# Kernel optimization log

Measured on AMD Instinct MI355X. Metric: run time of the kernel, lower is better.

The kernel has to match this reference:

```python
import math
import jax, jax.numpy as jnp
import numpy as np

SAMPLE_RATE = 24000
HARMONIC_NUM = 8
SINE_AMP = 0.1


def setup_inputs() -> dict:
    key = jax.random.key(0)
    k1, k2, k3 = jax.random.split(key, 3)
    f0 = jax.random.uniform(k1, (32, 800), dtype=jnp.float32)  # frame-rate F0
    W = jax.random.normal(k2, (9, 1), dtype=jnp.float32) * (1.0 / 3.0)  # Linear(9,1) weight
    b = jax.random.normal(k3, (1,), dtype=jnp.float32) * 0.01
    return {"f0": f0, "W": W, "b": b, "upp": 240}


def reference(f0, W, b, upp):
    # nearest-neighbor upsample by integer factor upp == repeat each frame
    f0_up = jnp.repeat(f0, upp, axis=1)  # [batch, samples]
    batch, samples = f0_up.shape
    # harmonic multipliers h = 1..harmonic_num+1 (9 harmonics)
    h = jnp.arange(1, HARMONIC_NUM + 2, dtype=f0.dtype)  # [9]
    # cumsum(f0_up * h) == cumsum(f0_up) * h (cumsum is linear); one scan for all harmonics
    base_phase = jnp.cumsum(f0_up / SAMPLE_RATE, axis=1)  # [batch, samples]
    phase = base_phase[:, :, None] * (h * (2.0 * math.pi))  # [batch, samples, 9]
    sine = jnp.sin(phase) * SINE_AMP
    uv = (f0_up > 0).astype(f0.dtype)[:, :, None]  # [batch, samples, 1]
    harmonics = sine * uv
    har_source = jnp.tanh(harmonics @ W + b)  # [batch, samples, 1]
    noise = jax.random.normal(jax.random.key(1234), (batch, samples, 1), dtype=f0.dtype) * (SINE_AMP / 3.0)
    return (har_source, noise, uv)
```

## Files before the change

### kernel.cpp

```cpp
#include <hip/hip_runtime.h>
#include <stdint.h>

#define FRAMES  800
#define UPP     240
#define SAMPLES (FRAMES * UPP)
#define BATCH   32
#define NTOT    (BATCH * SAMPLES)
#define NHALF   (NTOT / 2)

#define THREEFRY_PARTITIONABLE 1

__device__ __forceinline__ uint32_t rotl32(uint32_t v, int d) {
  return (v << d) | (v >> (32 - d));
}

__device__ __forceinline__ void threefry2x32(uint32_t k0, uint32_t k1,
                                             uint32_t x0, uint32_t x1,
                                             uint32_t& o0, uint32_t& o1) {
  const uint32_t ks0 = k0, ks1 = k1, ks2 = k0 ^ k1 ^ 0x1BD11BDAu;
  x0 += ks0; x1 += ks1;
#define TF_R(r) { x0 += x1; x1 = rotl32(x1, r); x1 ^= x0; }
  TF_R(13) TF_R(15) TF_R(26) TF_R(6)   x0 += ks1; x1 += ks2 + 1u;
  TF_R(17) TF_R(29) TF_R(16) TF_R(24)  x0 += ks2; x1 += ks0 + 2u;
  TF_R(13) TF_R(15) TF_R(26) TF_R(6)   x0 += ks0; x1 += ks1 + 3u;
  TF_R(17) TF_R(29) TF_R(16) TF_R(24)  x0 += ks1; x1 += ks2 + 4u;
  TF_R(13) TF_R(15) TF_R(26) TF_R(6)   x0 += ks2; x1 += ks0 + 5u;
#undef TF_R
  o0 = x0; o1 = x1;
}

__device__ __forceinline__ float erfinv_f32(float x) {
  float w = -log1pf(-x * x);
  float p;
  if (w < 5.0f) {
    w = w - 2.5f;
    p = 2.81022636e-08f;
    p = fmaf(p, w, 3.43273939e-07f);
    p = fmaf(p, w, -3.5233877e-06f);
    p = fmaf(p, w, -4.39150654e-06f);
    p = fmaf(p, w, 0.00021858087f);
    p = fmaf(p, w, -0.00125372503f);
    p = fmaf(p, w, -0.00417768164f);
    p = fmaf(p, w, 0.246640727f);
    p = fmaf(p, w, 1.50140941f);
  } else {
    w = sqrtf(w) - 3.0f;
    p = -0.000200214257f;
    p = fmaf(p, w, 0.000100950558f);
    p = fmaf(p, w, 0.00134934322f);
    p = fmaf(p, w, -0.00367342844f);
    p = fmaf(p, w, 0.00573950773f);
    p = fmaf(p, w, -0.0076224613f);
    p = fmaf(p, w, 0.00943887047f);
    p = fmaf(p, w, 1.00167406f);
    p = fmaf(p, w, 2.83297682f);
  }
  return p * x;
}

__device__ __forceinline__ float bits_to_noise(uint32_t bits) {
  float f = __uint_as_float((bits >> 9) | 0x3f800000u);
  float u = f - 1.0f;
  const float lo = -0.99999994f;
  float val = fmaf(u, 2.0f, lo);
  val = fmaxf(lo, val);
  float n = 1.41421356f * erfinv_f32(val);
  return n * 0.033333335f;
}

#if THREEFRY_PARTITIONABLE
__global__ __launch_bounds__(256) void noise_kernel(float* __restrict__ out) {
  uint32_t i0 = (blockIdx.x * 256u + threadIdx.x) * 4u;
  if (i0 >= (uint32_t)NTOT) return;
  float4 r;
  uint32_t a, b;
  threefry2x32(0u, 1234u, 0u, i0 + 0u, a, b); r.x = bits_to_noise(a ^ b);
  threefry2x32(0u, 1234u, 0u, i0 + 1u, a, b); r.y = bits_to_noise(a ^ b);
  threefry2x32(0u, 1234u, 0u, i0 + 2u, a, b); r.z = bits_to_noise(a ^ b);
  threefry2x32(0u, 1234u, 0u, i0 + 3u, a, b); r.w = bits_to_noise(a ^ b);
  *(float4*)(out + i0) = r;
}
#else
__global__ __launch_bounds__(256) void noise_kernel(float* __restrict__ out) {
  uint32_t p0 = (blockIdx.x * 256u + threadIdx.x) * 4u;
  if (p0 >= (uint32_t)NHALF) return;
  float4 rlo, rhi;
  uint32_t a, b;
  threefry2x32(0u, 1234u, p0 + 0u, p0 + 0u + (uint32_t)NHALF, a, b);
  rlo.x = bits_to_noise(a); rhi.x = bits_to_noise(b);
  threefry2x32(0u, 1234u, p0 + 1u, p0 + 1u + (uint32_t)NHALF, a, b);
  rlo.y = bits_to_noise(a); rhi.y = bits_to_noise(b);
  threefry2x32(0u, 1234u, p0 + 2u, p0 + 2u + (uint32_t)NHALF, a, b);
  rlo.z = bits_to_noise(a); rhi.z = bits_to_noise(b);
  threefry2x32(0u, 1234u, p0 + 3u, p0 + 3u + (uint32_t)NHALF, a, b);
  rlo.w = bits_to_noise(a); rhi.w = bits_to_noise(b);
  *(float4*)(out + p0) = rlo;
  *(float4*)(out + p0 + NHALF) = rhi;
}
#endif

__global__ __launch_bounds__(256) void har_uv_kernel(
    const float* __restrict__ f0, const float* __restrict__ W,
    const float* __restrict__ bptr, float* __restrict__ har,
    float* __restrict__ uv) {
  __shared__ float  sf0[FRAMES];
  __shared__ double sP[FRAMES];
  __shared__ double sScan[256];

  const int tid = threadIdx.x;
  const int row = blockIdx.y;
  const float* f0row = f0 + row * FRAMES;

  for (int i = tid; i < FRAMES; i += 256) sf0[i] = f0row[i];
  __syncthreads();

  const int fb = tid * 4;
  double v0 = 0.0, v1 = 0.0, v2 = 0.0, v3 = 0.0;
  if (fb < FRAMES) {
    v0 = (double)sf0[fb];     v1 = (double)sf0[fb + 1];
    v2 = (double)sf0[fb + 2]; v3 = (double)sf0[fb + 3];
  }
  const double tot = v0 + v1 + v2 + v3;
  sScan[tid] = tot;
  __syncthreads();
  for (int off = 1; off < 256; off <<= 1) {
    double add = (tid >= off) ? sScan[tid - off] : 0.0;
    __syncthreads();
    sScan[tid] += add;
    __syncthreads();
  }
  const double excl = (tid > 0) ? sScan[tid - 1] : 0.0;
  if (fb < FRAMES) {
    sP[fb]     = excl;
    sP[fb + 1] = excl + v0;
    sP[fb + 2] = excl + v0 + v1;
    sP[fb + 3] = excl + v0 + v1 + v2;
  }
  __syncthreads();

  const int t0 = (blockIdx.x * 256 + tid) * 4;
  if (t0 >= SAMPLES) return;

  float Wr[9];
#pragma unroll
  for (int h = 0; h < 9; ++h) Wr[h] = W[h];
  const float bias = bptr[0];

  const int frame = t0 / UPP;
  const int j = t0 - frame * UPP;
  const float fv = sf0[frame];
  const float amp = (fv > 0.0f) ? 0.1f : 0.0f;
  const float uvf = (fv > 0.0f) ? 1.0f : 0.0f;
  const double fp = sP[frame] * (double)UPP;
  const double fd = (double)fv;

  float hout[4];
#pragma unroll
  for (int k = 0; k < 4; ++k) {
    double ph = (fp + (double)(j + 1 + k) * fd) * (1.0 / 24000.0);
    double fr = ph - floor(ph);
    float f = (float)fr;
#if __has_builtin(__builtin_amdgcn_sinf)
    float s1 = __builtin_amdgcn_sinf(f);
    float c1 = __builtin_amdgcn_cosf(f);
#else
    float s1 = sinf(6.2831853f * f);
    float c1 = cosf(6.2831853f * f);
#endif
    float tc = 2.0f * c1;
    float skm1 = 0.0f, sk = s1;
    float dot = Wr[0] * s1;
#pragma unroll
    for (int h = 2; h <= 9; ++h) {
      float sn = tc * sk - skm1;
      skm1 = sk; sk = sn;
      dot = fmaf(Wr[h - 1], sn, dot);
    }
    hout[k] = tanhf(fmaf(amp, dot, bias));
  }

  const int base = row * SAMPLES + t0;
  *(float4*)(har + base) = make_float4(hout[0], hout[1], hout[2], hout[3]);
  *(float4*)(uv + base)  = make_float4(uvf, uvf, uvf, uvf);
}

extern "C" void kernel_launch(void* const* d_in, const int* in_sizes, int n_in,
                              void* d_out, int out_size, void* d_ws, size_t ws_size,
                              hipStream_t stream) {
  const float* f0 = (const float*)d_in[0];
  const float* W  = (const float*)d_in[1];
  const float* b  = (const float*)d_in[2];

  float* out   = (float*)d_out;
  float* har   = out;
  float* noise = out + NTOT;
  float* uvp   = out + 2 * NTOT;

#if THREEFRY_PARTITIONABLE
  noise_kernel<<<NTOT / 1024, 256, 0, stream>>>(noise);
#else
  noise_kernel<<<NHALF / 1024, 256, 0, stream>>>(noise);
#endif
  dim3 g((SAMPLES + 1023) / 1024, BATCH);
  har_uv_kernel<<<g, 256, 0, stream>>>(f0, W, b, har, uvp);
}
```

Baseline: 121.1 us.

## Split scan into own kernel and fuse noise generation into harmonic kernel

Moves the per-row double-precision prefix scan into a small separate kernel that writes the fractional frame phase (mod 1, using UPP/24000 = 0.01) to workspace. The main kernel then computes per-sample phase in fp32 from that fraction, fuses threefry noise generation into the same pass, and uses an exp/rcp tanh. This removes the redundant per-block scan, the per-sample fp64 math and a separate noise kernel launch. In exchange it adds an extra launch with a workspace round trip, and fp32 phase and the approximate tanh carry small precision risk.

```diff
diff --git a/kernel.cpp b/kernel.cpp
--- a/kernel.cpp
+++ b/kernel.cpp
@@ -6,9 +6,6 @@
 #define SAMPLES (FRAMES * UPP)
 #define BATCH   32
 #define NTOT    (BATCH * SAMPLES)
-#define NHALF   (NTOT / 2)
-
-#define THREEFRY_PARTITIONABLE 1
 
 __device__ __forceinline__ uint32_t rotl32(uint32_t v, int d) {
   return (v << d) | (v >> (32 - d));
@@ -68,60 +65,25 @@
   return n * 0.033333335f;
 }
 
-#if THREEFRY_PARTITIONABLE
-__global__ __launch_bounds__(256) void noise_kernel(float* __restrict__ out) {
-  uint32_t i0 = (blockIdx.x * 256u + threadIdx.x) * 4u;
-  if (i0 >= (uint32_t)NTOT) return;
-  float4 r;
-  uint32_t a, b;
-  threefry2x32(0u, 1234u, 0u, i0 + 0u, a, b); r.x = bits_to_noise(a ^ b);
-  threefry2x32(0u, 1234u, 0u, i0 + 1u, a, b); r.y = bits_to_noise(a ^ b);
-  threefry2x32(0u, 1234u, 0u, i0 + 2u, a, b); r.z = bits_to_noise(a ^ b);
-  threefry2x32(0u, 1234u, 0u, i0 + 3u, a, b); r.w = bits_to_noise(a ^ b);
-  *(float4*)(out + i0) = r;
+__device__ __forceinline__ float fast_tanhf(float x) {
+  float e = __expf(-2.0f * x);
+  return (1.0f - e) * __builtin_amdgcn_rcpf(1.0f + e);
 }
-#else
-__global__ __launch_bounds__(256) void noise_kernel(float* __restrict__ out) {
-  uint32_t p0 = (blockIdx.x * 256u + threadIdx.x) * 4u;
-  if (p0 >= (uint32_t)NHALF) return;
-  float4 rlo, rhi;
-  uint32_t a, b;
-  threefry2x32(0u, 1234u, p0 + 0u, p0 + 0u + (uint32_t)NHALF, a, b);
-  rlo.x = bits_to_noise(a); rhi.x = bits_to_noise(b);
-  threefry2x32(0u, 1234u, p0 + 1u, p0 + 1u + (uint32_t)NHALF, a, b);
-  rlo.y = bits_to_noise(a); rhi.y = bits_to_noise(b);
-  threefry2x32(0u, 1234u, p0 + 2u, p0 + 2u + (uint32_t)NHALF, a, b);
-  rlo.z = bits_to_noise(a); rhi.z = bits_to_noise(b);
-  threefry2x32(0u, 1234u, p0 + 3u, p0 + 3u + (uint32_t)NHALF, a, b);
-  rlo.w = bits_to_noise(a); rhi.w = bits_to_noise(b);
-  *(float4*)(out + p0) = rlo;
-  *(float4*)(out + p0 + NHALF) = rhi;
-}
-#endif
 
-__global__ __launch_bounds__(256) void har_uv_kernel(
-    const float* __restrict__ f0, const float* __restrict__ W,
-    const float* __restrict__ bptr, float* __restrict__ har,
-    float* __restrict__ uv) {
-  __shared__ float  sf0[FRAMES];
-  __shared__ double sP[FRAMES];
+__global__ __launch_bounds__(256) void scan_kernel(
+    const float* __restrict__ f0, float* __restrict__ pfrac) {
   __shared__ double sScan[256];
-
   const int tid = threadIdx.x;
-  const int row = blockIdx.y;
+  const int row = blockIdx.x;
   const float* f0row = f0 + row * FRAMES;
-
-  for (int i = tid; i < FRAMES; i += 256) sf0[i] = f0row[i];
-  __syncthreads();
 
   const int fb = tid * 4;
   double v0 = 0.0, v1 = 0.0, v2 = 0.0, v3 = 0.0;
   if (fb < FRAMES) {
-    v0 = (double)sf0[fb];     v1 = (double)sf0[fb + 1];
-    v2 = (double)sf0[fb + 2]; v3 = (double)sf0[fb + 3];
+    v0 = (double)f0row[fb];     v1 = (double)f0row[fb + 1];
+    v2 = (double)f0row[fb + 2]; v3 = (double)f0row[fb + 3];
   }
-  const double tot = v0 + v1 + v2 + v3;
-  sScan[tid] = tot;
+  sScan[tid] = v0 + v1 + v2 + v3;
   __syncthreads();
   for (int off = 1; off < 256; off <<= 1) {
     double add = (tid >= off) ? sScan[tid - off] : 0.0;
@@ -129,44 +91,52 @@
     sScan[tid] += add;
     __syncthreads();
   }
-  const double excl = (tid > 0) ? sScan[tid - 1] : 0.0;
   if (fb < FRAMES) {
-    sP[fb]     = excl;
-    sP[fb + 1] = excl + v0;
-    sP[fb + 2] = excl + v0 + v1;
-    sP[fb + 3] = excl + v0 + v1 + v2;
+    const double excl = (tid > 0) ? sScan[tid - 1] : 0.0;
+    double p0 = excl;
+    double p1 = excl + v0;
+    double p2 = excl + v0 + v1;
+    double p3 = excl + v0 + v1 + v2;
+    float* o = pfrac + row * FRAMES + fb;
+    double c0 = p0 * 0.01; o[0] = (float)(c0 - floor(c0));
+    double c1 = p1 * 0.01; o[1] = (float)(c1 - floor(c1));
+    double c2 = p2 * 0.01; o[2] = (float)(c2 - floor(c2));
+    double c3 = p3 * 0.01; o[3] = (float)(c3 - floor(c3));
   }
-  __syncthreads();
+}
 
-  const int t0 = (blockIdx.x * 256 + tid) * 4;
+__global__ __launch_bounds__(256) void fused_kernel(
+    const float* __restrict__ f0, const float* __restrict__ pfrac,
+    const float* __restrict__ W, const float* __restrict__ bptr,
+    float* __restrict__ out) {
+  const int t0 = (blockIdx.x * 256 + threadIdx.x) * 4;
   if (t0 >= SAMPLES) return;
+  const int row = blockIdx.y;
+
+  const int frame = t0 / UPP;
+  const int j = t0 - frame * UPP;
+  const float fv   = f0[row * FRAMES + frame];
+  const float pf   = pfrac[row * FRAMES + frame];
+  const float step = fv * (1.0f / 24000.0f);
+  const float amp  = (fv > 0.0f) ? 0.1f : 0.0f;
+  const float uvf  = (fv > 0.0f) ? 1.0f : 0.0f;
 
   float Wr[9];
 #pragma unroll
   for (int h = 0; h < 9; ++h) Wr[h] = W[h];
   const float bias = bptr[0];
 
-  const int frame = t0 / UPP;
-  const int j = t0 - frame * UPP;
-  const float fv = sf0[frame];
-  const float amp = (fv > 0.0f) ? 0.1f : 0.0f;
-  const float uvf = (fv > 0.0f) ? 1.0f : 0.0f;
-  const double fp = sP[frame] * (double)UPP;
-  const double fd = (double)fv;
+  const uint32_t gbase = (uint32_t)(row * SAMPLES + t0);
 
-  float hout[4];
+  float4 hv, nv;
+  float* hvp = &hv.x;
+  float* nvp = &nv.x;
 #pragma unroll
   for (int k = 0; k < 4; ++k) {
-    double ph = (fp + (double)(j + 1 + k) * fd) * (1.0 / 24000.0);
-    double fr = ph - floor(ph);
-    float f = (float)fr;
-#if __has_builtin(__builtin_amdgcn_sinf)
-    float s1 = __builtin_amdgcn_sinf(f);
-    float c1 = __builtin_amdgcn_cosf(f);
-#else
-    float s1 = sinf(6.2831853f * f);
-    float c1 = cosf(6.2831853f * f);
-#endif
+    float ph = fmaf((float)(j + 1 + k), step, pf);
+    ph -= (ph >= 1.0f) ? 1.0f : 0.0f;
+    float s1 = __builtin_amdgcn_sinf(ph);
+    float c1 = __builtin_amdgcn_cosf(ph);
     float tc = 2.0f * c1;
     float skm1 = 0.0f, sk = s1;
     float dot = Wr[0] * s1;
@@ -176,12 +146,19 @@
       skm1 = sk; sk = sn;
       dot = fmaf(Wr[h - 1], sn, dot);
     }
-    hout[k] = tanhf(fmaf(amp, dot, bias));
+    hvp[k] = fast_tanhf(fmaf(amp, dot, bias));
+
+    uint32_t a, b;
+    threefry2x32(0u, 1234u, 0u, gbase + (uint32_t)k, a, b);
+    nvp[k] = bits_to_noise(a ^ b);
   }
 
-  const int base = row * SAMPLES + t0;
-  *(float4*)(har + base) = make_float4(hout[0], hout[1], hout[2], hout[3]);
-  *(float4*)(uv + base)  = make_float4(uvf, uvf, uvf, uvf);
+  float* har   = out;
+  float* noise = out + NTOT;
+  float* uvp   = out + 2 * NTOT;
+  *(float4*)(har + gbase)   = hv;
+  *(float4*)(noise + gbase) = nv;
+  *(float4*)(uvp + gbase)   = make_float4(uvf, uvf, uvf, uvf);
 }
 
 extern "C" void kernel_launch(void* const* d_in, const int* in_sizes, int n_in,
@@ -191,16 +168,10 @@
   const float* W  = (const float*)d_in[1];
   const float* b  = (const float*)d_in[2];
 
+  float* pfrac = (float*)d_ws;
   float* out   = (float*)d_out;
-  float* har   = out;
-  float* noise = out + NTOT;
-  float* uvp   = out + 2 * NTOT;
 
-#if THREEFRY_PARTITIONABLE
-  noise_kernel<<<NTOT / 1024, 256, 0, stream>>>(noise);
-#else
-  noise_kernel<<<NHALF / 1024, 256, 0, stream>>>(noise);
-#endif
+  scan_kernel<<<BATCH, 256, 0, stream>>>(f0, pfrac);
   dim3 g((SAMPLES + 1023) / 1024, BATCH);
-  har_uv_kernel<<<g, 256, 0, stream>>>(f0, W, b, har, uvp);
+  fused_kernel<<<g, 256, 0, stream>>>(f0, pfrac, W, b, out);
 }
```

New measurement: 113.7 us. 1.06x faster.
